# Optimization experiments

Hardware: AMD Instinct MI355X
Metric: run time of the kernel (lower is better)

## Reference

```python
import jax, jax.numpy as jnp
from jax import lax
import numpy as np

B, T, D_IN, H, L, D_OUT = 1024, 512, 6, 128, 3, 1


def _lstm_layer(xs, w_ih, w_hh, b_ih, b_hh):
    """xs: [B, T, Din]; w_ih: [4H, Din]; w_hh: [4H, H]. PyTorch gate order i,f,g,o."""
    Bq = xs.shape[0]
    Hq = w_hh.shape[1]
    # Precompute the input projection for all timesteps (compute-dense part).
    x_proj = jnp.einsum('btd,gd->btg', xs, w_ih) + (b_ih + b_hh)  # [B, T, 4H]

    def step(carry, xp):
        h, c = carry
        gates = xp + h @ w_hh.T  # [B, 4H]
        i, f, g, o = jnp.split(gates, 4, axis=-1)
        i = jax.nn.sigmoid(i)
        f = jax.nn.sigmoid(f)
        g = jnp.tanh(g)
        o = jax.nn.sigmoid(o)
        c = f * c + i * g
        h = o * jnp.tanh(c)
        return (h, c), h

    h0 = jnp.zeros((Bq, Hq), xs.dtype)
    c0 = jnp.zeros((Bq, Hq), xs.dtype)
    (_, _), hs = lax.scan(step, (h0, c0), jnp.swapaxes(x_proj, 0, 1))  # hs: [T, B, H]
    return jnp.swapaxes(hs, 0, 1)  # [B, T, H]


def setup_inputs() -> dict:
    key = jax.random.key(0)
    ks = jax.random.split(key, 16)
    s = 1.0 / np.sqrt(H)  # PyTorch LSTM init scale
    inp = {"x": jax.random.normal(ks[0], (B, T, D_IN), dtype=jnp.float32)}
    din = D_IN
    for l in range(L):
        inp[f"w_ih{l}"] = jax.random.uniform(ks[1 + 4 * l], (4 * H, din), minval=-s, maxval=s, dtype=jnp.float32)
        inp[f"w_hh{l}"] = jax.random.uniform(ks[2 + 4 * l], (4 * H, H), minval=-s, maxval=s, dtype=jnp.float32)
        inp[f"b_ih{l}"] = jax.random.uniform(ks[3 + 4 * l], (4 * H,), minval=-s, maxval=s, dtype=jnp.float32)
        inp[f"b_hh{l}"] = jax.random.uniform(ks[4 + 4 * l], (4 * H,), minval=-s, maxval=s, dtype=jnp.float32)
        din = H
    inp["fc_w"] = jax.random.uniform(ks[13], (D_OUT, H), minval=-s, maxval=s, dtype=jnp.float32)
    inp["fc_b"] = jax.random.uniform(ks[14], (D_OUT,), minval=-s, maxval=s, dtype=jnp.float32)
    return inp


def reference(x, w_ih0, w_hh0, b_ih0, b_hh0, w_ih1, w_hh1, b_ih1, b_hh1,
              w_ih2, w_hh2, b_ih2, b_hh2, fc_w, fc_b):
    # 3-layer LSTM (inference: dropout between layers is identity) + final Linear on last timestep.
    h = _lstm_layer(x, w_ih0, w_hh0, b_ih0, b_hh0)
    h = _lstm_layer(h, w_ih1, w_hh1, b_ih1, b_hh1)
    h = _lstm_layer(h, w_ih2, w_hh2, b_ih2, b_hh2)
    return h[:, -1, :] @ fc_w.T + fc_b  # [B, 1]
```

## Files before the change

kernel.cpp:

```cpp
#include <hip/hip_runtime.h>

#define TLEN  512
#define HID   128
#define RSLOT 16

typedef __attribute__((ext_vector_type(8))) short          bf16x8;
typedef __attribute__((ext_vector_type(4))) float          f32x4;
typedef __attribute__((ext_vector_type(4))) unsigned short u16x4;
typedef unsigned long long u64;

#define LOG2E  1.4426950408889634f
#define LOG2E2 2.8853900817779268f

__device__ __forceinline__ unsigned short f2bf(float f) {
    union { float f; unsigned u; } v; v.f = f;
    unsigned r = v.u + 0x7fffu + ((v.u >> 16) & 1u);
    return (unsigned short)(r >> 16);
}
__device__ __forceinline__ unsigned short f2bf_fast(float f) {
    union { float f; unsigned u; } v; v.f = f;
    return (unsigned short)((v.u + 0x8000u) >> 16);
}

__device__ __forceinline__ float sig_ps(float xs) {
    return __builtin_amdgcn_rcpf(1.0f + __builtin_exp2f(-xs));
}
__device__ __forceinline__ float tanh_ps(float xs) {
    return 2.0f * __builtin_amdgcn_rcpf(1.0f + __builtin_exp2f(-xs)) - 1.0f;
}

__device__ __forceinline__ int flag_peek(const int* f) {
    return __hip_atomic_load(f, __ATOMIC_RELAXED, __HIP_MEMORY_SCOPE_AGENT);
}
__device__ __forceinline__ int flag_spin(const int* f, int v) {
    int x = flag_peek(f);
    while (x < v) { __builtin_amdgcn_s_sleep(1); x = flag_peek(f); }
    return x;
}
__device__ __forceinline__ void flag_pub(int* f, int v) {
    __hip_atomic_store(f, v, __ATOMIC_RELAXED, __HIP_MEMORY_SCOPE_WORKGROUP);
}

template<int MODE, bool CONS, bool PROD, bool WFC>
__device__ __forceinline__ void run_layer_p(
    const float* __restrict__ xin,
    const u64* __restrict__ rin, u64* __restrict__ rout,
    const int* pin_flag, int* cout_flag, const int* cin_flag, int* pout_flag,
    const float* __restrict__ wih, const float* __restrict__ whh,
    const float* __restrict__ bih, const float* __restrict__ bhh,
    unsigned short (* __restrict__ hbuf)[2048],
    unsigned short (* __restrict__ xbuf)[2048],
    float* __restrict__ fcred,
    const int tid, const int wave, const int lane,
    const int n16, const int quad, const int bbase)
{
    constexpr int NKTX = MODE ? 4 : 1;
    constexpr int DINL = MODE ? 128 : 6;

    bf16x8 Wfx[4][NKTX], Wfh[4][4];
    float  bb[4];
#pragma unroll
    for (int g = 0; g < 4; ++g) {
        const float sc = (g == 2) ? LOG2E2 : LOG2E;
        const int row = g * 128 + wave * 16 + n16;
        bb[g] = (bih[row] + bhh[row]) * sc;
#pragma unroll
        for (int kt = 0; kt < NKTX; ++kt) {
            bf16x8 wv;
#pragma unroll
            for (int j = 0; j < 8; ++j) {
                const int k = kt * 32 + quad * 8 + j;
                wv[j] = (short)f2bf(((k < DINL) ? wih[row * DINL + k] : 0.0f) * sc);
            }
            Wfx[g][kt] = wv;
        }
#pragma unroll
        for (int kt = 0; kt < 4; ++kt) {
            bf16x8 wv;
#pragma unroll
            for (int j = 0; j < 8; ++j) {
                const int k = kt * 32 + quad * 8 + j;
                wv[j] = (short)f2bf(whh[row * HID + k] * sc);
            }
            Wfh[g][kt] = wv;
        }
    }

    { u16x4 z = {0, 0, 0, 0}; *(u16x4*)&hbuf[0][tid * 4] = z; }
    u64 q0 = 0, q1 = 0, q2 = 0, qn = 0;
    float pfx0 = 0.0f;
    int pend = 0, cpend = 0;
    const int xm = tid >> 5, xk = tid & 31;
    if constexpr (CONS) {
        flag_spin(pin_flag, 1);
        *(u64*)&xbuf[0][tid * 4] =
            __hip_atomic_load(rin + tid, __ATOMIC_RELAXED, __HIP_MEMORY_SCOPE_AGENT);
        flag_spin(pin_flag, 2);
        *(u64*)&xbuf[1][tid * 4] =
            __hip_atomic_load(rin + 512 + tid, __ATOMIC_RELAXED, __HIP_MEMORY_SCOPE_AGENT);
        pend = flag_spin(pin_flag, 5);
        q0 = __hip_atomic_load(rin + 2 * 512 + tid, __ATOMIC_RELAXED, __HIP_MEMORY_SCOPE_AGENT);
        q1 = __hip_atomic_load(rin + 3 * 512 + tid, __ATOMIC_RELAXED, __HIP_MEMORY_SCOPE_AGENT);
        q2 = __hip_atomic_load(rin + 4 * 512 + tid, __ATOMIC_RELAXED, __HIP_MEMORY_SCOPE_AGENT);
    } else {
        const int ei = ((xk >> 3) * 16 + xm) * 8 + (xk & 7);
        float v0 = (xk < DINL) ? xin[((bbase + xm) * TLEN + 0) * DINL + xk] : 0.0f;
        float v1 = (xk < DINL) ? xin[((bbase + xm) * TLEN + 1) * DINL + xk] : 0.0f;
        xbuf[0][ei] = f2bf(v0);
        xbuf[1][ei] = f2bf(v1);
        if (xk < DINL) pfx0 = xin[((bbase + xm) * TLEN + 2) * DINL + xk];
    }
    if constexpr (PROD) cpend = -(1 << 30);
    __syncthreads();

    f32x4 accA[4], accB[4];
#pragma unroll
    for (int g = 0; g < 4; ++g) { f32x4 bi = {bb[g], bb[g], bb[g], bb[g]}; accA[g] = bi; }
#pragma unroll
    for (int kt = 0; kt < NKTX; ++kt) {
        bf16x8 a = *(const bf16x8*)&xbuf[0][kt * 512 + lane * 8];
#pragma unroll
        for (int g = 0; g < 4; ++g)
            accA[g] = __builtin_amdgcn_mfma_f32_16x16x32_bf16(a, Wfx[g][kt], accA[g], 0, 0, 0);
    }

    float cst[4] = {0.f, 0.f, 0.f, 0.f};
    int rd = 1, wr = 2;

    auto step = [&](f32x4 (&accC)[4], f32x4 (&accN)[4], int t) {
        const int cur = t & 1, nxt = cur ^ 1;
        __syncthreads();

        if constexpr (CONS) {
            if (t + 5 < TLEN) {
                if (pend < t + 6) pend = flag_spin(pin_flag, t + 6);
                qn = __hip_atomic_load(rin + ((t + 5) & (RSLOT - 1)) * 512 + tid,
                                       __ATOMIC_RELAXED, __HIP_MEMORY_SCOPE_AGENT);
                pend = flag_peek(pin_flag);
            }
        }
        if (tid == 0) {
            if constexpr (CONS) if ((t & 3) == 0) flag_pub(cout_flag, t + 5);
            if constexpr (PROD) if (t >= 2)       flag_pub(pout_flag, t - 1);
        }
        if constexpr (PROD) {
            if (t >= 1) {
                const int e = t - 1;
                if ((e & 3) == 0 && e + 4 > RSLOT && cpend < e + 4 - RSLOT)
                    cpend = flag_spin(cin_flag, e + 4 - RSLOT);
                u64 hv = *(const u64*)&hbuf[cur][tid * 4];
                __hip_atomic_store(rout + (e & (RSLOT - 1)) * 512 + tid, hv,
                                   __ATOMIC_RELAXED, __HIP_MEMORY_SCOPE_WORKGROUP);
                if ((e & 3) == 1) cpend = flag_peek(cin_flag);
            }
        }
        float pfx1 = 0.0f;
        if constexpr (!CONS) {
            if (t + 3 < TLEN && xk < DINL)
                pfx1 = xin[((bbase + xm) * TLEN + (t + 3)) * DINL + xk];
        }

#pragma unroll
        for (int kt = 0; kt < 4; ++kt) {
            bf16x8 a = *(const bf16x8*)&hbuf[cur][kt * 512 + lane * 8];
#pragma unroll
            for (int g = 0; g < 4; ++g)
                accC[g] = __builtin_amdgcn_mfma_f32_16x16x32_bf16(a, Wfh[g][kt], accC[g], 0, 0, 0);
        }

        if (t + 1 < TLEN) {
#pragma unroll
            for (int g = 0; g < 4; ++g) { f32x4 bi = {bb[g], bb[g], bb[g], bb[g]}; accN[g] = bi; }
#pragma unroll
            for (int kt = 0; kt < NKTX; ++kt) {
                bf16x8 a = *(const bf16x8*)&xbuf[rd][kt * 512 + lane * 8];
#pragma unroll
                for (int g = 0; g < 4; ++g)
                    accN[g] = __builtin_amdgcn_mfma_f32_16x16x32_bf16(a, Wfx[g][kt], accN[g], 0, 0, 0);
            }
        }

        unsigned short hb[4]; float hf[4];
#pragma unroll
        for (int r = 0; r < 4; ++r) {
            const float iv = sig_ps (accC[0][r]);
            const float fv = sig_ps (accC[1][r]);
            const float gv = tanh_ps(accC[2][r]);
            const float ov = sig_ps (accC[3][r]);
            const float c  = fv * cst[r] + iv * gv;
            cst[r] = c;
            const float h  = ov * tanh_ps(c * LOG2E2);
            hf[r] = h;
            hb[r] = f2bf_fast(h);
        }
        {
            const int j  = wave * 16 + n16;
            const int eb = (j >> 5) * 512 + (((j & 31) >> 3) * 16) * 8 + ((j & 31) & 7);
#pragma unroll
            for (int r = 0; r < 4; ++r)
                hbuf[nxt][eb + (quad * 4 + r) * 8] = hb[r];
        }
        if constexpr (WFC) {
            if (t == TLEN - 1)
#pragma unroll
                for (int r = 0; r < 4; ++r)
                    fcred[(quad * 4 + r) * HID + wave * 16 + n16] = hf[r];
        }
        if (t + 2 < TLEN) {
            if constexpr (CONS) {
                *(u64*)&xbuf[wr][tid * 4] = q0;
                q0 = q1; q1 = q2; q2 = qn;
            } else {
                xbuf[wr][((xk >> 3) * 16 + xm) * 8 + (xk & 7)] = f2bf(pfx0);
                pfx0 = pfx1;
            }
        }
        rd = wr; wr = (wr == 2) ? 0 : wr + 1;
    };

    for (int t = 0; t < TLEN; t += 2) {
        step(accA, accB, t);
        step(accB, accA, t + 1);
    }

    if constexpr (PROD) {
        __syncthreads();
        if (tid == 0) flag_pub(pout_flag, TLEN - 1);
        {
            flag_spin(cin_flag, TLEN - RSLOT);
            u64 hv = *(const u64*)&hbuf[TLEN & 1][tid * 4];
            __hip_atomic_store(rout + ((TLEN - 1) & (RSLOT - 1)) * 512 + tid, hv,
                               __ATOMIC_RELAXED, __HIP_MEMORY_SCOPE_WORKGROUP);
        }
        __syncthreads();
        if (tid == 0) flag_pub(pout_flag, TLEN);
    }
}

extern "C" __global__ __launch_bounds__(512, 1)
void lstm3_pipe_kernel(const float* __restrict__ xin,
    const float* __restrict__ wih0, const float* __restrict__ whh0,
    const float* __restrict__ bih0, const float* __restrict__ bhh0,
    const float* __restrict__ wih1, const float* __restrict__ whh1,
    const float* __restrict__ bih1, const float* __restrict__ bhh1,
    const float* __restrict__ wih2, const float* __restrict__ whh2,
    const float* __restrict__ bih2, const float* __restrict__ bhh2,
    const float* __restrict__ fcw, const float* __restrict__ fcb,
    float* __restrict__ out,
    int* __restrict__ flags, u64* __restrict__ ring0, u64* __restrict__ ring1)
{
    __shared__ unsigned short hbuf[2][2048];
    __shared__ unsigned short xbuf[3][2048];
    __shared__ float fcred[16 * HID];

    const int tid   = threadIdx.x;
    const int wave  = tid >> 6;
    const int lane  = tid & 63;
    const int n16   = lane & 15;
    const int quad  = lane >> 4;

    const int xcd    = blockIdx.x & 7;
    const int grp    = blockIdx.x >> 3;
    const int layer  = grp % 3;
    const int sgroup = grp / 3;
    const int slice  = sgroup * 8 + xcd;
    const int bbase  = slice * 16;

    u64* r0 = ring0 + (size_t)slice * (RSLOT * 512);
    u64* r1 = ring1 + (size_t)slice * (RSLOT * 512);
    int* prod0 = flags + (size_t)(0 * 64 + slice) * 64;
    int* prod1 = flags + (size_t)(1 * 64 + slice) * 64;
    int* cons1 = flags + (size_t)(2 * 64 + slice) * 64;
    int* cons2 = flags + (size_t)(3 * 64 + slice) * 64;

    if (layer == 0) {
        run_layer_p<0, false, true, false>(xin, nullptr, r0,
            nullptr, nullptr, cons1, prod0,
            wih0, whh0, bih0, bhh0, hbuf, xbuf, fcred, tid, wave, lane, n16, quad, bbase);
    } else if (layer == 1) {
        run_layer_p<1, true, true, false>(nullptr, r0, r1,
            prod0, cons1, cons2, prod1,
            wih1, whh1, bih1, bhh1, hbuf, xbuf, fcred, tid, wave, lane, n16, quad, bbase);
    } else {
        run_layer_p<1, true, false, true>(nullptr, r1, nullptr,
            prod1, cons2, nullptr, nullptr,
            wih2, whh2, bih2, bhh2, hbuf, xbuf, fcred, tid, wave, lane, n16, quad, bbase);
        __syncthreads();
        if (tid < 16) {
            float s = 0.0f;
#pragma unroll 8
            for (int j = 0; j < HID; ++j) s += fcw[j] * fcred[tid * HID + j];
            out[bbase + tid] = s + fcb[0];
        }
    }
}

extern "C" void kernel_launch(void* const* d_in, const int* in_sizes, int n_in,
                              void* d_out, int out_size, void* d_ws, size_t ws_size,
                              hipStream_t stream) {
    (void)in_sizes; (void)n_in; (void)out_size; (void)ws_size;
    const float* x    = (const float*)d_in[0];
    const float* wih0 = (const float*)d_in[1];
    const float* whh0 = (const float*)d_in[2];
    const float* bih0 = (const float*)d_in[3];
    const float* bhh0 = (const float*)d_in[4];
    const float* wih1 = (const float*)d_in[5];
    const float* whh1 = (const float*)d_in[6];
    const float* bih1 = (const float*)d_in[7];
    const float* bhh1 = (const float*)d_in[8];
    const float* wih2 = (const float*)d_in[9];
    const float* whh2 = (const float*)d_in[10];
    const float* bih2 = (const float*)d_in[11];
    const float* bhh2 = (const float*)d_in[12];
    const float* fcw  = (const float*)d_in[13];
    const float* fcb  = (const float*)d_in[14];
    float* out = (float*)d_out;

    int* flags = (int*)d_ws;
    u64* ring0 = (u64*)((char*)d_ws + 65536);
    u64* ring1 = ring0 + (size_t)64 * RSLOT * 512;

    lstm3_pipe_kernel<<<dim3(192), dim3(512), 0, stream>>>(
        x, wih0, whh0, bih0, bhh0, wih1, whh1, bih1, bhh1,
        wih2, whh2, bih2, bhh2, fcw, fcb, out, flags, ring0, ring1);
}
```

Measured before the change: 833.6 us.

## Pair timesteps in inter-layer ring and interleave input MFMAs with gate activations

The inter-layer ring now holds pairs of timesteps per slot, and each pair moves as one 16-byte store. Flag publishing and consumer fetches happen only on even steps, which halves the number of global ring transactions and flag operations. The next step's input-projection MFMAs are split and interleaved between the two halves of the gate activation math, so matrix and vector work can overlap. The bias is also fed directly as the MFMA accumulator input. The extra queue registers raise register pressure, and the two-step publish granularity adds one step of latency between layers.

```diff
diff --git a/kernel.cpp b/kernel.cpp
--- a/kernel.cpp
+++ b/kernel.cpp
@@ -2,12 +2,13 @@
 
 #define TLEN  512
 #define HID   128
-#define RSLOT 16
+#define PSLOT 16
 
 typedef __attribute__((ext_vector_type(8))) short          bf16x8;
 typedef __attribute__((ext_vector_type(4))) float          f32x4;
 typedef __attribute__((ext_vector_type(4))) unsigned short u16x4;
 typedef unsigned long long u64;
+typedef __attribute__((ext_vector_type(2))) unsigned long long u64x2;
 
 #define LOG2E  1.4426950408889634f
 #define LOG2E2 2.8853900817779268f
@@ -39,6 +40,9 @@
 }
 __device__ __forceinline__ void flag_pub(int* f, int v) {
     __hip_atomic_store(f, v, __ATOMIC_RELAXED, __HIP_MEMORY_SCOPE_WORKGROUP);
+}
+__device__ __forceinline__ u64 ring_ld(const u64* p) {
+    return __hip_atomic_load(p, __ATOMIC_RELAXED, __HIP_MEMORY_SCOPE_AGENT);
 }
 
 template<int MODE, bool CONS, bool PROD, bool WFC>
@@ -58,12 +62,14 @@
     constexpr int DINL = MODE ? 128 : 6;
 
     bf16x8 Wfx[4][NKTX], Wfh[4][4];
-    float  bb[4];
+    f32x4  bbreg[4];
 #pragma unroll
     for (int g = 0; g < 4; ++g) {
         const float sc = (g == 2) ? LOG2E2 : LOG2E;
         const int row = g * 128 + wave * 16 + n16;
-        bb[g] = (bih[row] + bhh[row]) * sc;
+        const float b = (bih[row] + bhh[row]) * sc;
+        f32x4 bi = {b, b, b, b};
+        bbreg[g] = bi;
 #pragma unroll
         for (int kt = 0; kt < NKTX; ++kt) {
             bf16x8 wv;
@@ -87,21 +93,19 @@
     }
 
     { u16x4 z = {0, 0, 0, 0}; *(u16x4*)&hbuf[0][tid * 4] = z; }
-    u64 q0 = 0, q1 = 0, q2 = 0, qn = 0;
+    u64 q0 = 0, q1 = 0, q2 = 0, q3 = 0, q4 = 0, qn0 = 0, qn1 = 0;
     float pfx0 = 0.0f;
     int pend = 0, cpend = 0;
     const int xm = tid >> 5, xk = tid & 31;
     if constexpr (CONS) {
         flag_spin(pin_flag, 1);
-        *(u64*)&xbuf[0][tid * 4] =
-            __hip_atomic_load(rin + tid, __ATOMIC_RELAXED, __HIP_MEMORY_SCOPE_AGENT);
-        flag_spin(pin_flag, 2);
-        *(u64*)&xbuf[1][tid * 4] =
-            __hip_atomic_load(rin + 512 + tid, __ATOMIC_RELAXED, __HIP_MEMORY_SCOPE_AGENT);
-        pend = flag_spin(pin_flag, 5);
-        q0 = __hip_atomic_load(rin + 2 * 512 + tid, __ATOMIC_RELAXED, __HIP_MEMORY_SCOPE_AGENT);
-        q1 = __hip_atomic_load(rin + 3 * 512 + tid, __ATOMIC_RELAXED, __HIP_MEMORY_SCOPE_AGENT);
-        q2 = __hip_atomic_load(rin + 4 * 512 + tid, __ATOMIC_RELAXED, __HIP_MEMORY_SCOPE_AGENT);
+        *(u64*)&xbuf[0][tid * 4] = ring_ld(rin + tid * 2);
+        *(u64*)&xbuf[1][tid * 4] = ring_ld(rin + tid * 2 + 1);
+        pend = flag_spin(pin_flag, 3);
+        q0 = ring_ld(rin + 1 * 1024 + tid * 2);
+        q1 = ring_ld(rin + 1 * 1024 + tid * 2 + 1);
+        q2 = ring_ld(rin + 2 * 1024 + tid * 2);
+        q3 = ring_ld(rin + 2 * 1024 + tid * 2 + 1);
     } else {
         const int ei = ((xk >> 3) * 16 + xm) * 8 + (xk & 7);
         float v0 = (xk < DINL) ? xin[((bbase + xm) * TLEN + 0) * DINL + xk] : 0.0f;
@@ -115,45 +119,46 @@
 
     f32x4 accA[4], accB[4];
 #pragma unroll
-    for (int g = 0; g < 4; ++g) { f32x4 bi = {bb[g], bb[g], bb[g], bb[g]}; accA[g] = bi; }
-#pragma unroll
     for (int kt = 0; kt < NKTX; ++kt) {
         bf16x8 a = *(const bf16x8*)&xbuf[0][kt * 512 + lane * 8];
 #pragma unroll
         for (int g = 0; g < 4; ++g)
-            accA[g] = __builtin_amdgcn_mfma_f32_16x16x32_bf16(a, Wfx[g][kt], accA[g], 0, 0, 0);
+            accA[g] = __builtin_amdgcn_mfma_f32_16x16x32_bf16(
+                a, Wfx[g][kt], kt == 0 ? bbreg[g] : accA[g], 0, 0, 0);
     }
 
     float cst[4] = {0.f, 0.f, 0.f, 0.f};
     int rd = 1, wr = 2;
 
-    auto step = [&](f32x4 (&accC)[4], f32x4 (&accN)[4], int t) {
+    auto step = [&](f32x4 (&accC)[4], f32x4 (&accN)[4], int t, int PAR) {
         const int cur = t & 1, nxt = cur ^ 1;
         __syncthreads();
 
-        if constexpr (CONS) {
-            if (t + 5 < TLEN) {
-                if (pend < t + 6) pend = flag_spin(pin_flag, t + 6);
-                qn = __hip_atomic_load(rin + ((t + 5) & (RSLOT - 1)) * 512 + tid,
-                                       __ATOMIC_RELAXED, __HIP_MEMORY_SCOPE_AGENT);
-                pend = flag_peek(pin_flag);
-            }
-        }
-        if (tid == 0) {
-            if constexpr (CONS) if ((t & 3) == 0) flag_pub(cout_flag, t + 5);
-            if constexpr (PROD) if (t >= 2)       flag_pub(pout_flag, t - 1);
-        }
-        if constexpr (PROD) {
-            if (t >= 1) {
-                const int e = t - 1;
-                if ((e & 3) == 0 && e + 4 > RSLOT && cpend < e + 4 - RSLOT)
-                    cpend = flag_spin(cin_flag, e + 4 - RSLOT);
-                u64 hv = *(const u64*)&hbuf[cur][tid * 4];
-                __hip_atomic_store(rout + (e & (RSLOT - 1)) * 512 + tid, hv,
-                                   __ATOMIC_RELAXED, __HIP_MEMORY_SCOPE_WORKGROUP);
-                if ((e & 3) == 1) cpend = flag_peek(cin_flag);
-            }
-        }
+        if (PAR == 0) {
+            if constexpr (CONS) {
+                if (t + 6 < TLEN) {
+                    const int need = (t + 8) >> 1;
+                    if (pend < need) pend = flag_spin(pin_flag, need);
+                    const u64* rp = rin + (((t + 6) >> 1) & (PSLOT - 1)) * 1024 + tid * 2;
+                    qn0 = ring_ld(rp);
+                    qn1 = ring_ld(rp + 1);
+                    pend = flag_peek(pin_flag);
+                }
+                if (tid == 0 && (t & 3) == 0) flag_pub(cout_flag, t + 6);
+            }
+            if constexpr (PROD) {
+                if (tid == 0 && t >= 4) flag_pub(pout_flag, (t - 2) >> 1);
+                if (t >= 2) {
+                    if (t >= 34 && cpend < t - 33) cpend = flag_spin(cin_flag, t - 33);
+                    u64x2 hv;
+                    hv.x = *(const u64*)&hbuf[nxt][tid * 4];
+                    hv.y = *(const u64*)&hbuf[cur][tid * 4];
+                    *(u64x2*)(rout + ((((t - 2) >> 1) & (PSLOT - 1)) * 1024 + tid * 2)) = hv;
+                    if ((t & 3) == 2) cpend = flag_peek(cin_flag);
+                }
+            }
+        }
+
         float pfx1 = 0.0f;
         if constexpr (!CONS) {
             if (t + 3 < TLEN && xk < DINL)
@@ -168,21 +173,9 @@
                 accC[g] = __builtin_amdgcn_mfma_f32_16x16x32_bf16(a, Wfh[g][kt], accC[g], 0, 0, 0);
         }
 
-        if (t + 1 < TLEN) {
-#pragma unroll
-            for (int g = 0; g < 4; ++g) { f32x4 bi = {bb[g], bb[g], bb[g], bb[g]}; accN[g] = bi; }
-#pragma unroll
-            for (int kt = 0; kt < NKTX; ++kt) {
-                bf16x8 a = *(const bf16x8*)&xbuf[rd][kt * 512 + lane * 8];
-#pragma unroll
-                for (int g = 0; g < 4; ++g)
-                    accN[g] = __builtin_amdgcn_mfma_f32_16x16x32_bf16(a, Wfx[g][kt], accN[g], 0, 0, 0);
-            }
-        }
-
         unsigned short hb[4]; float hf[4];
 #pragma unroll
-        for (int r = 0; r < 4; ++r) {
+        for (int r = 0; r < 2; ++r) {
             const float iv = sig_ps (accC[0][r]);
             const float fv = sig_ps (accC[1][r]);
             const float gv = tanh_ps(accC[2][r]);
@@ -190,9 +183,43 @@
             const float c  = fv * cst[r] + iv * gv;
             cst[r] = c;
             const float h  = ov * tanh_ps(c * LOG2E2);
-            hf[r] = h;
-            hb[r] = f2bf_fast(h);
-        }
+            hf[r] = h; hb[r] = f2bf_fast(h);
+        }
+
+        const bool has_n = (t + 1 < TLEN);
+        if (has_n) {
+#pragma unroll
+            for (int kt = 0; kt < (NKTX > 1 ? 2 : 1); ++kt) {
+                bf16x8 a = *(const bf16x8*)&xbuf[rd][kt * 512 + lane * 8];
+#pragma unroll
+                for (int g = 0; g < 4; ++g)
+                    accN[g] = __builtin_amdgcn_mfma_f32_16x16x32_bf16(
+                        a, Wfx[g][kt], kt == 0 ? bbreg[g] : accN[g], 0, 0, 0);
+            }
+        }
+
+#pragma unroll
+        for (int r = 2; r < 4; ++r) {
+            const float iv = sig_ps (accC[0][r]);
+            const float fv = sig_ps (accC[1][r]);
+            const float gv = tanh_ps(accC[2][r]);
+            const float ov = sig_ps (accC[3][r]);
+            const float c  = fv * cst[r] + iv * gv;
+            cst[r] = c;
+            const float h  = ov * tanh_ps(c * LOG2E2);
+            hf[r] = h; hb[r] = f2bf_fast(h);
+        }
+
+        if (has_n && NKTX > 1) {
+#pragma unroll
+            for (int kt = 2; kt < NKTX; ++kt) {
+                bf16x8 a = *(const bf16x8*)&xbuf[rd][kt * 512 + lane * 8];
+#pragma unroll
+                for (int g = 0; g < 4; ++g)
+                    accN[g] = __builtin_amdgcn_mfma_f32_16x16x32_bf16(a, Wfx[g][kt], accN[g], 0, 0, 0);
+            }
+        }
+
         {
             const int j  = wave * 16 + n16;
             const int eb = (j >> 5) * 512 + (((j & 31) >> 3) * 16) * 8 + ((j & 31) & 7);
@@ -206,10 +233,13 @@
                 for (int r = 0; r < 4; ++r)
                     fcred[(quad * 4 + r) * HID + wave * 16 + n16] = hf[r];
         }
+
         if (t + 2 < TLEN) {
             if constexpr (CONS) {
+                if (PAR == 1) { q3 = qn0; q4 = qn1; }
                 *(u64*)&xbuf[wr][tid * 4] = q0;
-                q0 = q1; q1 = q2; q2 = qn;
+                q0 = q1; q1 = q2; q2 = q3;
+                if (PAR == 1) q3 = q4;
             } else {
                 xbuf[wr][((xk >> 3) * 16 + xm) * 8 + (xk & 7)] = f2bf(pfx0);
                 pfx0 = pfx1;
@@ -219,21 +249,22 @@
     };
 
     for (int t = 0; t < TLEN; t += 2) {
-        step(accA, accB, t);
-        step(accB, accA, t + 1);
+        step(accA, accB, t, 0);
+        step(accB, accA, t + 1, 1);
     }
 
     if constexpr (PROD) {
         __syncthreads();
-        if (tid == 0) flag_pub(pout_flag, TLEN - 1);
+        if (tid == 0) flag_pub(pout_flag, (TLEN - 2) >> 1);
         {
-            flag_spin(cin_flag, TLEN - RSLOT);
-            u64 hv = *(const u64*)&hbuf[TLEN & 1][tid * 4];
-            __hip_atomic_store(rout + ((TLEN - 1) & (RSLOT - 1)) * 512 + tid, hv,
-                               __ATOMIC_RELAXED, __HIP_MEMORY_SCOPE_WORKGROUP);
+            flag_spin(cin_flag, TLEN - 33);
+            u64x2 hv;
+            hv.x = *(const u64*)&hbuf[1][tid * 4];
+            hv.y = *(const u64*)&hbuf[0][tid * 4];
+            *(u64x2*)(rout + ((((TLEN - 2) >> 1) & (PSLOT - 1)) * 1024 + tid * 2)) = hv;
         }
         __syncthreads();
-        if (tid == 0) flag_pub(pout_flag, TLEN);
+        if (tid == 0) flag_pub(pout_flag, TLEN >> 1);
     }
 }
 
@@ -266,8 +297,8 @@
     const int slice  = sgroup * 8 + xcd;
     const int bbase  = slice * 16;
 
-    u64* r0 = ring0 + (size_t)slice * (RSLOT * 512);
-    u64* r1 = ring1 + (size_t)slice * (RSLOT * 512);
+    u64* r0 = ring0 + (size_t)slice * (PSLOT * 1024);
+    u64* r1 = ring1 + (size_t)slice * (PSLOT * 1024);
     int* prod0 = flags + (size_t)(0 * 64 + slice) * 64;
     int* prod1 = flags + (size_t)(1 * 64 + slice) * 64;
     int* cons1 = flags + (size_t)(2 * 64 + slice) * 64;
@@ -318,7 +349,7 @@
 
     int* flags = (int*)d_ws;
     u64* ring0 = (u64*)((char*)d_ws + 65536);
-    u64* ring1 = ring0 + (size_t)64 * RSLOT * 512;
+    u64* ring1 = ring0 + (size_t)64 * PSLOT * 1024;
 
     lstm3_pipe_kernel<<<dim3(192), dim3(512), 0, stream>>>(
         x, wih0, whh0, bih0, bhh0, wih1, whh1, bih1, bhh1,
```

Result: slower. 857.3 us (+2.8%).
